# Kernel optimization log

Measured on AMD Instinct MI355X. Metric: run time of the kernel, lower is better.

The kernel has to match this reference:

```python
import jax, jax.numpy as jnp
import numpy as np

WINDOW_SIZE = 2
SOFTMAX_TEMP = 0.01
WIDTH = 320
EPS = 1e-12  # F.normalize default eps


def _l2norm(x, axis):
    n = jnp.sqrt(jnp.sum(x * x, axis=axis, keepdims=True))
    return x / jnp.maximum(n, EPS)


def setup_inputs() -> dict:
    key = jax.random.key(0)
    k1, k2, k3, k4 = jax.random.split(key, 4)
    BW, C, N, S = 4, 256, 1024, 1
    return {
        "keypoint_scores": jax.random.uniform(k1, (BW, S, N), dtype=jnp.float32),
        "keypoint_desc": jax.random.normal(k2, (BW, C, N), dtype=jnp.float32),
        "desc_dense": jax.random.normal(k3, (BW, C, WIDTH, WIDTH), dtype=jnp.float32),
        "keypoint_coords": jax.random.uniform(k4, (BW, N, 2), dtype=jnp.float32),
    }


def reference(keypoint_scores, keypoint_desc, desc_dense, keypoint_coords):
    BW, C, N = keypoint_desc.shape
    B = BW // WINDOW_SIZE
    P = B * (WINDOW_SIZE - 1)  # number of (src, tgt) pairs

    # dense source pixel coordinates (u=col, v=row), matching torch meshgrid 'ij'
    idx = jnp.arange(WIDTH * WIDTH)
    coords = jnp.stack([(idx % WIDTH).astype(jnp.float32),
                        (idx // WIDTH).astype(jnp.float32)], axis=1)  # (HW, 2)

    # pair indexing: for window i, targets are i*w+1 .. i*w+w-1, source is i*w
    tgt_ids = jnp.array([i * WINDOW_SIZE + j for i in range(B)
                         for j in range(1, WINDOW_SIZE)], dtype=jnp.int32)
    src_ids = (tgt_ids // WINDOW_SIZE) * WINDOW_SIZE

    # normalized dense source descriptors: (B, C, HW)
    src_dense = desc_dense[::WINDOW_SIZE].reshape(B, C, -1)
    src_un = _l2norm(src_dense, axis=1)
    src_sel = src_un[tgt_ids // WINDOW_SIZE]  # (P, C, HW)

    # normalized target keypoint descriptors: (P, C, N)
    tgt_n = _l2norm(keypoint_desc[tgt_ids], axis=1)

    # QK^T over descriptor channel: (P, N, HW)
    match_vals = jnp.einsum('pcn,pcm->pnm', tgt_n, src_sel)
    soft = jax.nn.softmax(match_vals / SOFTMAX_TEMP, axis=2)

    # soft-argmax coordinates: (P, N, 2)
    pseudo_coords = jnp.einsum('pnm,md->pnd', soft, coords)

    match_weights = keypoint_scores[tgt_ids]  # (P, S, N)
    return pseudo_coords, match_weights, tgt_ids, src_ids
```

## Files before the change

### kernel.cpp

```cpp
#include <hip/hip_runtime.h>
#include <stdint.h>

#define HW_      102400
#define C_       256
#define N_       1024
#define P_       2
#define TILES_   1600
#define CHUNKS_  32
#define ITERS_   50
#define NB_      4
#define K2_      144.269504088896340f
#define MOFF_    (-72.134752044448170f)

typedef __attribute__((ext_vector_type(8))) short bf16x8;
typedef __attribute__((ext_vector_type(4))) float f32x4;

#define WS_TGT_OFF  0
#define WS_PAR_OFF  (1u << 20)
#define WS_PN_OFF   (4u << 20)

__device__ __forceinline__ uint32_t packbf(float a, float b) {
  uint32_t r;
  asm("v_cvt_pk_bf16_f32 %0, %1, %2" : "=v"(r) : "v"(a), "v"(b));
  return r;
}
__device__ __forceinline__ float fexp2(float x) {
  return __builtin_amdgcn_exp2f(x);
}

__global__ __launch_bounds__(256)
void k_pre(const float* __restrict__ dense, const float* __restrict__ kdesc,
           const float* __restrict__ kscores, uint32_t* __restrict__ PN,
           uint16_t* __restrict__ tgt, float* __restrict__ out) {
  __shared__ float part[16][64];
  __shared__ float sinv[64];
  const int bid = blockIdx.x;
  if (bid < P_ * TILES_) {
    const int p = bid / TILES_, tile = bid % TILES_;
    const int t   = threadIdx.x;
    const int px4 = (t & 15) * 4;
    const int cg  = t >> 4;
    const float* src = dense + (size_t)(p * 2) * C_ * HW_ + (size_t)(cg * 16) * HW_
                     + tile * 64 + px4;
    float v[16][4];
    #pragma unroll
    for (int cc = 0; cc < 16; ++cc) {
      const float4 q = *(const float4*)(src + (size_t)cc * HW_);
      v[cc][0] = q.x; v[cc][1] = q.y; v[cc][2] = q.z; v[cc][3] = q.w;
    }
    float ps[4] = {0.f, 0.f, 0.f, 0.f};
    #pragma unroll
    for (int cc = 0; cc < 16; ++cc) {
      #pragma unroll
      for (int i = 0; i < 4; ++i) ps[i] = fmaf(v[cc][i], v[cc][i], ps[i]);
    }
    #pragma unroll
    for (int i = 0; i < 4; ++i) part[cg][px4 + i] = ps[i];
    __syncthreads();
    if (t < 64) {
      float s = 0.f;
      #pragma unroll
      for (int g = 0; g < 16; ++g) s += part[g][t];
      sinv[t] = 1.f / fmaxf(sqrtf(s), 1e-12f);
    }
    __syncthreads();
    uint32_t* dstg = PN + ((size_t)(p * TILES_ + tile) << 13);
    const int kk   = cg >> 1;
    const int half = cg & 1;
    #pragma unroll
    for (int i = 0; i < 4; ++i) {
      const int r  = px4 + i;
      const float iv = sinv[r];
      uint32_t* d = dstg + (kk * 64 + r) * 16 + half * 8;
      uint4 A, B;
      A.x = packbf(v[0][i] * iv,  v[1][i] * iv);
      A.y = packbf(v[2][i] * iv,  v[3][i] * iv);
      A.z = packbf(v[4][i] * iv,  v[5][i] * iv);
      A.w = packbf(v[6][i] * iv,  v[7][i] * iv);
      B.x = packbf(v[8][i] * iv,  v[9][i] * iv);
      B.y = packbf(v[10][i] * iv, v[11][i] * iv);
      B.z = packbf(v[12][i] * iv, v[13][i] * iv);
      B.w = packbf(v[14][i] * iv, v[15][i] * iv);
      *(uint4*)&d[0] = A;
      *(uint4*)&d[4] = B;
    }
  } else {
    const int t = (bid - P_ * TILES_) * 256 + threadIdx.x;
    const int p = t >> 10, n = t & 1023;
    const float* src = kdesc + (size_t)(p * 2 + 1) * C_ * N_ + n;
    float s = 0.f;
    #pragma unroll 16
    for (int c = 0; c < C_; ++c) { const float v2 = src[c * N_]; s = fmaf(v2, v2, s); }
    const float inv = 1.f / fmaxf(sqrtf(s), 1e-12f);
    uint32_t* dst = (uint32_t*)(tgt + (size_t)t * C_);
    #pragma unroll 4
    for (int c8 = 0; c8 < C_; c8 += 8) {
      uint4 wv;
      wv.x = packbf(src[(c8 + 0) * N_] * inv, src[(c8 + 1) * N_] * inv);
      wv.y = packbf(src[(c8 + 2) * N_] * inv, src[(c8 + 3) * N_] * inv);
      wv.z = packbf(src[(c8 + 4) * N_] * inv, src[(c8 + 5) * N_] * inv);
      wv.w = packbf(src[(c8 + 6) * N_] * inv, src[(c8 + 7) * N_] * inv);
      *(uint4*)&dst[c8 / 2] = wv;
    }
    out[4096 + t] = kscores[(p * 2 + 1) * N_ + n];
  }
}

__global__ __launch_bounds__(512, 2)
void k_main(const uint32_t* __restrict__ PN, const uint16_t* __restrict__ tgt,
            float4* __restrict__ partials) {
  const int bid = blockIdx.x;
  const int xcd = bid & 7;
  const int rr  = bid >> 3;
  const int nb  = rr & 3;
  const int grp = xcd + 8 * (rr >> 2);
  const int p     = grp >> 5;
  const int chunk = grp & 31;

  const int t    = threadIdx.x;
  const int lane = t & 63;
  const int w    = t >> 6;
  const int l15  = lane & 15;
  const int g4   = lane >> 4;
  const int h    = w & 1;
  const int q    = w >> 1;

  bf16x8 Bf[4][8];
  const int nbase = nb * 256 + q * 64;
  #pragma unroll
  for (int j = 0; j < 4; ++j) {
    const uint16_t* tp = tgt + (size_t)(p * N_ + nbase + j * 16 + l15) * C_ + g4 * 8;
    #pragma unroll
    for (int k = 0; k < 8; ++k) Bf[j][k] = *(const bf16x8*)(tp + k * 32);
  }

  float stS[4], stU[4], stV[4];
  #pragma unroll
  for (int j = 0; j < 4; ++j) { stS[j] = 0.f; stU[j] = 0.f; stV[j] = 0.f; }

  const int lr0 = h * 32 + g4 * 4;
  const int aoff = (h * 32 + l15) * 16 + g4 * 4;

  float offf[2][4];
  #pragma unroll
  for (int s = 0; s < 2; ++s)
    #pragma unroll
    for (int e = 0; e < 4; ++e) offf[s][e] = (float)(lr0 + s * 16 + e);

  const uint32_t* PNc = PN + ((size_t)(p * TILES_ + chunk * ITERS_) << 13);

  float u0f = 0.f, v0f = (float)(chunk * 10);
  for (int iter = 0; iter < ITERS_; ++iter) {
    const uint32_t* bt = PNc + ((size_t)iter << 13);

    f32x4 acc[4][2];
    #pragma unroll
    for (int j = 0; j < 4; ++j) {
      acc[j][0] = (f32x4){0.f, 0.f, 0.f, 0.f};
      acc[j][1] = (f32x4){0.f, 0.f, 0.f, 0.f};
    }
    __builtin_amdgcn_s_setprio(1);
    #pragma unroll
    for (int k = 0; k < 8; ++k) {
      const bf16x8 a0 = *(const bf16x8*)&bt[k * 1024 + aoff];
      const bf16x8 a1 = *(const bf16x8*)&bt[k * 1024 + 256 + aoff];
      acc[0][0] = __builtin_amdgcn_mfma_f32_16x16x32_bf16(a0, Bf[0][k], acc[0][0], 0, 0, 0);
      acc[0][1] = __builtin_amdgcn_mfma_f32_16x16x32_bf16(a1, Bf[0][k], acc[0][1], 0, 0, 0);
      acc[1][0] = __builtin_amdgcn_mfma_f32_16x16x32_bf16(a0, Bf[1][k], acc[1][0], 0, 0, 0);
      acc[1][1] = __builtin_amdgcn_mfma_f32_16x16x32_bf16(a1, Bf[1][k], acc[1][1], 0, 0, 0);
      acc[2][0] = __builtin_amdgcn_mfma_f32_16x16x32_bf16(a0, Bf[2][k], acc[2][0], 0, 0, 0);
      acc[2][1] = __builtin_amdgcn_mfma_f32_16x16x32_bf16(a1, Bf[2][k], acc[2][1], 0, 0, 0);
      acc[3][0] = __builtin_amdgcn_mfma_f32_16x16x32_bf16(a0, Bf[3][k], acc[3][0], 0, 0, 0);
      acc[3][1] = __builtin_amdgcn_mfma_f32_16x16x32_bf16(a1, Bf[3][k], acc[3][1], 0, 0, 0);
    }
    __builtin_amdgcn_s_setprio(0);

    #pragma unroll
    for (int j = 0; j < 4; ++j) {
      float tS = 0.f, tU = 0.f;
      #pragma unroll
      for (int s = 0; s < 2; ++s) {
        #pragma unroll
        for (int e = 0; e < 4; ++e) {
          const float ev = fexp2(fmaf(K2_, acc[j][s][e], MOFF_));
          tS += ev;
          tU = fmaf(ev, offf[s][e], tU);
        }
      }
      stS[j] += tS;
      stU[j] += fmaf(u0f, tS, tU);
      stV[j] = fmaf(v0f, tS, stV[j]);
    }
    u0f += 64.f;
    if (u0f > 290.f) { u0f = 0.f; v0f += 1.f; }
  }

  #pragma unroll
  for (int j = 0; j < 4; ++j) {
    float S = stS[j], U = stU[j], V = stV[j];
    S += __shfl_xor(S, 16, 64); U += __shfl_xor(U, 16, 64); V += __shfl_xor(V, 16, 64);
    S += __shfl_xor(S, 32, 64); U += __shfl_xor(U, 32, 64); V += __shfl_xor(V, 32, 64);
    if (lane < 16) {
      const int n = nbase + j * 16 + l15;
      partials[((size_t)(p * CHUNKS_ + chunk) * 2 + h) * N_ + n] = make_float4(S, U, V, 0.f);
    }
  }
}

__global__ void k_final(const float4* __restrict__ partials, float* __restrict__ out) {
  const int t = blockIdx.x * blockDim.x + threadIdx.x;
  const int p = t >> 10, n = t & 1023;
  float S = 0.f, U = 0.f, V = 0.f;
  #pragma unroll 4
  for (int s = 0; s < 2 * CHUNKS_; ++s) {
    const float4 v = partials[((size_t)p * 2 * CHUNKS_ + s) * N_ + n];
    S += v.x; U += v.y; V += v.z;
  }
  out[(size_t)(p * N_ + n) * 2 + 0] = U / S;
  out[(size_t)(p * N_ + n) * 2 + 1] = V / S;
  if (t < 4) {
    const float ids[4] = {1.f, 3.f, 0.f, 2.f};
    out[6144 + t] = ids[t];
  }
}

extern "C" void kernel_launch(void* const* d_in, const int* in_sizes, int n_in,
                              void* d_out, int out_size, void* d_ws, size_t ws_size,
                              hipStream_t stream) {
  const float* kscores = (const float*)d_in[0];
  const float* kdesc   = (const float*)d_in[1];
  const float* dense   = (const float*)d_in[2];
  float* out = (float*)d_out;

  char* ws = (char*)d_ws;
  uint16_t* tgt = (uint16_t*)(ws + WS_TGT_OFF);
  float4*   par = (float4*)(ws + WS_PAR_OFF);
  uint32_t* PN  = (uint32_t*)(ws + WS_PN_OFF);

  k_pre<<<P_ * TILES_ + (P_ * N_) / 256, 256, 0, stream>>>(dense, kdesc, kscores, PN, tgt, out);
  k_main<<<P_ * NB_ * CHUNKS_, 512, 0, stream>>>(PN, tgt, par);
  k_final<<<(P_ * N_) / 256, 256, 0, stream>>>(par, out);
}
```

Measured before the change: 219.5 us.

## Switch main GEMM to 32x32x16 MFMA with double-buffered LDS DMA staging

Rearranges the packed normalized dense descriptor layout so that k_main can use 32x32x16 bf16 MFMAs instead of 16x16x32. Tiles are now brought in two at a time through global_load_lds into a double-buffered shared-memory area, prefetching the next pair while the current one is computed. The softmax-weighted coordinate reduction is reworked to match the 32x32 accumulator layout. This aims to raise MFMA efficiency and hide global load latency, at the cost of 128KB of LDS per block, which may reduce occupancy from the declared two blocks per CU, plus an extra barrier per pair of tiles.

```diff
diff --git a/kernel.cpp b/kernel.cpp
--- a/kernel.cpp
+++ b/kernel.cpp
@@ -7,13 +7,13 @@
 #define P_       2
 #define TILES_   1600
 #define CHUNKS_  32
-#define ITERS_   50
+#define MEGAS_   25
 #define NB_      4
 #define K2_      144.269504088896340f
 #define MOFF_    (-72.134752044448170f)
 
-typedef __attribute__((ext_vector_type(8))) short bf16x8;
-typedef __attribute__((ext_vector_type(4))) float f32x4;
+typedef __attribute__((ext_vector_type(8)))  short bf16x8;
+typedef __attribute__((ext_vector_type(16))) float f32x16;
 
 #define WS_TGT_OFF  0
 #define WS_PAR_OFF  (1u << 20)
@@ -26,6 +26,11 @@
 }
 __device__ __forceinline__ float fexp2(float x) {
   return __builtin_amdgcn_exp2f(x);
+}
+__device__ __forceinline__ void dma16(const uint32_t* g, uint32_t* l) {
+  __builtin_amdgcn_global_load_lds(
+      (const __attribute__((address_space(1))) uint32_t*)g,
+      (__attribute__((address_space(3))) uint32_t*)l, 16, 0, 0);
 }
 
 __global__ __launch_bounds__(256)
@@ -45,8 +50,8 @@
     float v[16][4];
     #pragma unroll
     for (int cc = 0; cc < 16; ++cc) {
-      const float4 q = *(const float4*)(src + (size_t)cc * HW_);
-      v[cc][0] = q.x; v[cc][1] = q.y; v[cc][2] = q.z; v[cc][3] = q.w;
+      const float4 qd = *(const float4*)(src + (size_t)cc * HW_);
+      v[cc][0] = qd.x; v[cc][1] = qd.y; v[cc][2] = qd.z; v[cc][3] = qd.w;
     }
     float ps[4] = {0.f, 0.f, 0.f, 0.f};
     #pragma unroll
@@ -64,14 +69,12 @@
       sinv[t] = 1.f / fmaxf(sqrtf(s), 1e-12f);
     }
     __syncthreads();
-    uint32_t* dstg = PN + ((size_t)(p * TILES_ + tile) << 13);
-    const int kk   = cg >> 1;
-    const int half = cg & 1;
+    uint32_t* dstg = PN + ((size_t)(p * TILES_ + tile) << 13) + cg * 512;
     #pragma unroll
     for (int i = 0; i < 4; ++i) {
       const int r  = px4 + i;
       const float iv = sinv[r];
-      uint32_t* d = dstg + (kk * 64 + r) * 16 + half * 8;
+      uint32_t* d = dstg + 4 * r;
       uint4 A, B;
       A.x = packbf(v[0][i] * iv,  v[1][i] * iv);
       A.y = packbf(v[2][i] * iv,  v[3][i] * iv);
@@ -81,8 +84,8 @@
       B.y = packbf(v[10][i] * iv, v[11][i] * iv);
       B.z = packbf(v[12][i] * iv, v[13][i] * iv);
       B.w = packbf(v[14][i] * iv, v[15][i] * iv);
-      *(uint4*)&d[0] = A;
-      *(uint4*)&d[4] = B;
+      *(uint4*)&d[0]   = A;
+      *(uint4*)&d[256] = B;
     }
   } else {
     const int t = (bid - P_ * TILES_) * 256 + threadIdx.x;
@@ -109,6 +112,8 @@
 __global__ __launch_bounds__(512, 2)
 void k_main(const uint32_t* __restrict__ PN, const uint16_t* __restrict__ tgt,
             float4* __restrict__ partials) {
+  __shared__ uint32_t lds[2 * 16384];
+
   const int bid = blockIdx.x;
   const int xcd = bid & 7;
   const int rr  = bid >> 3;
@@ -120,88 +125,93 @@
   const int t    = threadIdx.x;
   const int lane = t & 63;
   const int w    = t >> 6;
-  const int l15  = lane & 15;
-  const int g4   = lane >> 4;
+  const int l31  = lane & 31;
+  const int hi   = lane >> 5;
   const int h    = w & 1;
   const int q    = w >> 1;
 
-  bf16x8 Bf[4][8];
+  bf16x8 Bf[2][16];
   const int nbase = nb * 256 + q * 64;
   #pragma unroll
-  for (int j = 0; j < 4; ++j) {
-    const uint16_t* tp = tgt + (size_t)(p * N_ + nbase + j * 16 + l15) * C_ + g4 * 8;
-    #pragma unroll
-    for (int k = 0; k < 8; ++k) Bf[j][k] = *(const bf16x8*)(tp + k * 32);
-  }
-
-  float stS[4], stU[4], stV[4];
-  #pragma unroll
-  for (int j = 0; j < 4; ++j) { stS[j] = 0.f; stU[j] = 0.f; stV[j] = 0.f; }
-
-  const int lr0 = h * 32 + g4 * 4;
-  const int aoff = (h * 32 + l15) * 16 + g4 * 4;
-
-  float offf[2][4];
-  #pragma unroll
-  for (int s = 0; s < 2; ++s)
-    #pragma unroll
-    for (int e = 0; e < 4; ++e) offf[s][e] = (float)(lr0 + s * 16 + e);
-
-  const uint32_t* PNc = PN + ((size_t)(p * TILES_ + chunk * ITERS_) << 13);
+  for (int j = 0; j < 2; ++j) {
+    const uint16_t* tp = tgt + (size_t)(p * N_ + nbase + j * 32 + l31) * C_ + hi * 8;
+    #pragma unroll
+    for (int kk = 0; kk < 16; ++kk) Bf[j][kk] = *(const bf16x8*)(tp + kk * 16);
+  }
+
+  float stS[2], stU[2], stV[2];
+  #pragma unroll
+  for (int j = 0; j < 2; ++j) { stS[j] = 0.f; stU[j] = 0.f; stV[j] = 0.f; }
+
+  const int arow = hi * 256 + (h * 32 + l31) * 4;
+  const float ubstat = (float)(h * 32 + 4 * hi);
+
+  const uint32_t* PNc = PN + ((size_t)(p * TILES_ + chunk * 2 * MEGAS_) << 13) + w * 2048 + lane * 4;
+  uint32_t* ldsw = &lds[w * 2048];
+
+  #pragma unroll
+  for (int jj = 0; jj < 8; ++jj) dma16(PNc + jj * 256, ldsw + jj * 256);
+  __syncthreads();
 
   float u0f = 0.f, v0f = (float)(chunk * 10);
-  for (int iter = 0; iter < ITERS_; ++iter) {
-    const uint32_t* bt = PNc + ((size_t)iter << 13);
-
-    f32x4 acc[4][2];
-    #pragma unroll
-    for (int j = 0; j < 4; ++j) {
-      acc[j][0] = (f32x4){0.f, 0.f, 0.f, 0.f};
-      acc[j][1] = (f32x4){0.f, 0.f, 0.f, 0.f};
-    }
+  for (int m = 0; m < MEGAS_; ++m) {
+    if (m + 1 < MEGAS_) {
+      const uint32_t* s = PNc + ((size_t)(m + 1) << 14);
+      uint32_t* d = ldsw + (((m + 1) & 1) ? 16384 : 0);
+      #pragma unroll
+      for (int jj = 0; jj < 8; ++jj) dma16(s + jj * 256, d + jj * 256);
+    }
+
+    const uint32_t* buf = &lds[(m & 1) * 16384];
+    f32x16 acc[2][2];
+    #pragma unroll
+    for (int s2 = 0; s2 < 2; ++s2)
+      #pragma unroll
+      for (int j = 0; j < 2; ++j)
+        #pragma unroll
+        for (int e = 0; e < 16; ++e) acc[s2][j][e] = 0.f;
+
     __builtin_amdgcn_s_setprio(1);
     #pragma unroll
-    for (int k = 0; k < 8; ++k) {
-      const bf16x8 a0 = *(const bf16x8*)&bt[k * 1024 + aoff];
-      const bf16x8 a1 = *(const bf16x8*)&bt[k * 1024 + 256 + aoff];
-      acc[0][0] = __builtin_amdgcn_mfma_f32_16x16x32_bf16(a0, Bf[0][k], acc[0][0], 0, 0, 0);
-      acc[0][1] = __builtin_amdgcn_mfma_f32_16x16x32_bf16(a1, Bf[0][k], acc[0][1], 0, 0, 0);
-      acc[1][0] = __builtin_amdgcn_mfma_f32_16x16x32_bf16(a0, Bf[1][k], acc[1][0], 0, 0, 0);
-      acc[1][1] = __builtin_amdgcn_mfma_f32_16x16x32_bf16(a1, Bf[1][k], acc[1][1], 0, 0, 0);
-      acc[2][0] = __builtin_amdgcn_mfma_f32_16x16x32_bf16(a0, Bf[2][k], acc[2][0], 0, 0, 0);
-      acc[2][1] = __builtin_amdgcn_mfma_f32_16x16x32_bf16(a1, Bf[2][k], acc[2][1], 0, 0, 0);
-      acc[3][0] = __builtin_amdgcn_mfma_f32_16x16x32_bf16(a0, Bf[3][k], acc[3][0], 0, 0, 0);
-      acc[3][1] = __builtin_amdgcn_mfma_f32_16x16x32_bf16(a1, Bf[3][k], acc[3][1], 0, 0, 0);
+    for (int kk = 0; kk < 16; ++kk) {
+      const bf16x8 a0 = *(const bf16x8*)&buf[kk * 512 + arow];
+      const bf16x8 a1 = *(const bf16x8*)&buf[8192 + kk * 512 + arow];
+      acc[0][0] = __builtin_amdgcn_mfma_f32_32x32x16_bf16(a0, Bf[0][kk], acc[0][0], 0, 0, 0);
+      acc[0][1] = __builtin_amdgcn_mfma_f32_32x32x16_bf16(a0, Bf[1][kk], acc[0][1], 0, 0, 0);
+      acc[1][0] = __builtin_amdgcn_mfma_f32_32x32x16_bf16(a1, Bf[0][kk], acc[1][0], 0, 0, 0);
+      acc[1][1] = __builtin_amdgcn_mfma_f32_32x32x16_bf16(a1, Bf[1][kk], acc[1][1], 0, 0, 0);
     }
     __builtin_amdgcn_s_setprio(0);
 
     #pragma unroll
-    for (int j = 0; j < 4; ++j) {
-      float tS = 0.f, tU = 0.f;
-      #pragma unroll
-      for (int s = 0; s < 2; ++s) {
+    for (int s2 = 0; s2 < 2; ++s2) {
+      const float ub = u0f + ubstat;
+      #pragma unroll
+      for (int j = 0; j < 2; ++j) {
+        float tS = 0.f, tC = 0.f;
         #pragma unroll
-        for (int e = 0; e < 4; ++e) {
-          const float ev = fexp2(fmaf(K2_, acc[j][s][e], MOFF_));
+        for (int r = 0; r < 16; ++r) {
+          const float ev = fexp2(fmaf(K2_, acc[s2][j][r], MOFF_));
           tS += ev;
-          tU = fmaf(ev, offf[s][e], tU);
+          tC = fmaf(ev, (float)((r & 3) + 8 * (r >> 2)), tC);
         }
+        stS[j] += tS;
+        stU[j] = fmaf(ub, tS, stU[j] + tC);
+        stV[j] = fmaf(v0f, tS, stV[j]);
       }
-      stS[j] += tS;
-      stU[j] += fmaf(u0f, tS, tU);
-      stV[j] = fmaf(v0f, tS, stV[j]);
-    }
-    u0f += 64.f;
-    if (u0f > 290.f) { u0f = 0.f; v0f += 1.f; }
-  }
-
-  #pragma unroll
-  for (int j = 0; j < 4; ++j) {
+      u0f += 64.f;
+      if (u0f > 290.f) { u0f = 0.f; v0f += 1.f; }
+    }
+
+    __syncthreads();
+  }
+
+  #pragma unroll
+  for (int j = 0; j < 2; ++j) {
     float S = stS[j], U = stU[j], V = stV[j];
-    S += __shfl_xor(S, 16, 64); U += __shfl_xor(U, 16, 64); V += __shfl_xor(V, 16, 64);
     S += __shfl_xor(S, 32, 64); U += __shfl_xor(U, 32, 64); V += __shfl_xor(V, 32, 64);
-    if (lane < 16) {
-      const int n = nbase + j * 16 + l15;
+    if (lane < 32) {
+      const int n = nbase + j * 32 + l31;
       partials[((size_t)(p * CHUNKS_ + chunk) * 2 + h) * N_ + n] = make_float4(S, U, V, 0.f);
     }
   }
```

After: 189.7 us. 1.16x faster.
